# Kernel optimization log

Measured on AMD Instinct MI355X. Metric: run time of the kernel, lower is better.

Reference implementation:

```python
import jax, jax.numpy as jnp
import numpy as np

B, L, C, H, Wd = 256, 64, 256, 32, 32  # batch, num_filts, code_dim, height, width

def setup_inputs() -> dict:
    key = jax.random.key(0)
    k1, k2 = jax.random.split(key)
    code = jax.random.normal(k1, (B, L, C), dtype=jnp.float32)
    # stacked per-filter weights: weights[l].weight has shape [code_dim, H*W]
    W = jax.random.normal(k2, (L, C, H * Wd), dtype=jnp.float32) * (1.0 / np.sqrt(C))
    return {"code": code, "W": W}

def reference(code, W):
    # Original: for each filter l, x_hat[:, l] = code[:, l, :] @ weights[l].weight
    # (F.linear(x, weight.t()) == x @ weight). Fuse into one batched GEMM.
    # code: [B, L, C], W: [L, C, HW] -> out: [B, L, HW]
    x_hat = jnp.einsum('blc,lcd->bld', code, W)
    return x_hat.reshape(code.shape[0], W.shape[0], H, Wd)
```

## Files before the change

### kernel.cpp

```cpp
#include <hip/hip_runtime.h>
#include <hip/hip_bf16.h>

#define B_  256
#define L_  64
#define C_  256
#define HW_ 1024

typedef float  floatx4 __attribute__((ext_vector_type(4)));
typedef __bf16 bf16x8  __attribute__((ext_vector_type(8)));
typedef __bf16 bf16x4  __attribute__((ext_vector_type(4)));

#define LDT_A 72
#define LDB_ROW 128

#define BARRIER_LDS() asm volatile("s_waitcnt lgkmcnt(0)\n\ts_barrier" ::: "memory")

__device__ __forceinline__ int bswz(int n) { return (n ^ (n >> 2)) & 7; }

__global__ __launch_bounds__(512, 4)
void gld_mfma_kernel(const float* __restrict__ code,
                     const float* __restrict__ W,
                     float* __restrict__ out)
{
    const int tid = threadIdx.x;

    const int id  = blockIdx.x;
    const int ll  = id & 7;
    const int inr = id >> 3;
    const int m0  = (inr & 1) * 128;
    const int n0  = ((inr >> 1) & 7) * 128;
    const int l   = (inr >> 4) * 8 + ll;

    __shared__ __bf16 Alds[128 * LDT_A];
    __shared__ unsigned char Blds[128 * LDB_ROW];

    const int lane = tid & 63;
    const int wave = tid >> 6;
    const int wm = (wave >> 2) * 64;
    const int wn = (wave & 3) * 32;

    floatx4 acc[4][2];
    #pragma unroll
    for (int i = 0; i < 4; ++i)
        #pragma unroll
        for (int j = 0; j < 2; ++j)
            acc[i][j] = (floatx4)0.0f;

    const int a_row = tid >> 4;
    const int a_kc  = (tid & 15) * 4;
    const int b_i  = tid & 31;
    const int b_c8 = tid >> 5;

    const float* aBase = code + (size_t)m0 * (L_ * C_) + (size_t)l * C_ + a_kc;
    const float* wBase = W + (size_t)l * (C_ * HW_) + (size_t)(4 * b_c8) * HW_ + n0 + 4 * b_i;

    floatx4 Areg[2][4];
    floatx4 Breg[2][4];

    #pragma unroll
    for (int p = 0; p < 4; ++p)
        Areg[0][p] = *(const floatx4*)(aBase + (size_t)(p * 32 + a_row) * (L_ * C_));
    #pragma unroll
    for (int r = 0; r < 4; ++r)
        Breg[0][r] = *(const floatx4*)(wBase + (size_t)r * HW_);
    #pragma unroll
    for (int r = 0; r < 4; ++r)
        Breg[1][r] = *(const floatx4*)(wBase + (size_t)(64 + r) * HW_);

    int bwaddr[4];
    #pragma unroll
    for (int j = 0; j < 4; ++j) {
        const int row = 4 * b_i + j;
        bwaddr[j] = row * LDB_ROW + (((b_c8 >> 1) ^ bswz(row)) << 4) + ((b_c8 & 1) << 3);
    }

    #pragma unroll
    for (int kb = 0; kb < C_; kb += 64) {
        const int pp = (kb >> 6) & 1;

        if (kb + 64 < C_) {
            #pragma unroll
            for (int p = 0; p < 4; ++p)
                Areg[pp ^ 1][p] = *(const floatx4*)(aBase + (size_t)(p * 32 + a_row) * (L_ * C_) + (kb + 64));
        }

        #pragma unroll
        for (int j = 0; j < 4; ++j) {
            bf16x4 h;
            h.x = (__bf16)Breg[pp][0][j]; h.y = (__bf16)Breg[pp][1][j];
            h.z = (__bf16)Breg[pp][2][j]; h.w = (__bf16)Breg[pp][3][j];
            *(bf16x4*)&Blds[bwaddr[j]] = h;
        }

        if (kb + 128 < C_) {
            #pragma unroll
            for (int r = 0; r < 4; ++r)
                Breg[pp][r] = *(const floatx4*)(wBase + (size_t)(kb + 128 + r) * HW_);
        }

        #pragma unroll
        for (int p = 0; p < 4; ++p) {
            bf16x4 h;
            h.x = (__bf16)Areg[pp][p].x; h.y = (__bf16)Areg[pp][p].y;
            h.z = (__bf16)Areg[pp][p].z; h.w = (__bf16)Areg[pp][p].w;
            *(bf16x4*)&Alds[(p * 32 + a_row) * LDT_A + a_kc] = h;
        }

        BARRIER_LDS();

        #pragma unroll
        for (int ks = 0; ks < 2; ++ks) {
            bf16x8 af[4], bfr[2];
            const int koff = ks * 32 + (lane >> 4) * 8;
            #pragma unroll
            for (int i = 0; i < 4; ++i)
                af[i] = *(const bf16x8*)&Alds[(wm + i * 16 + (lane & 15)) * LDT_A + koff];
            #pragma unroll
            for (int j = 0; j < 2; ++j) {
                const int n = wn + j * 16 + (lane & 15);
                bfr[j] = *(const bf16x8*)&Blds[n * LDB_ROW + (((koff >> 3) ^ bswz(n)) << 4)];
            }
            #pragma unroll
            for (int i = 0; i < 4; ++i)
                #pragma unroll
                for (int j = 0; j < 2; ++j)
                    acc[i][j] = __builtin_amdgcn_mfma_f32_16x16x32_bf16(af[i], bfr[j], acc[i][j], 0, 0, 0);
        }

        BARRIER_LDS();
    }

    const int col0 = lane & 15;
    const int row0 = (lane >> 4) * 4;
    #pragma unroll
    for (int i = 0; i < 4; ++i) {
        #pragma unroll
        for (int j = 0; j < 2; ++j) {
            const int m = m0 + wm + i * 16 + row0;
            const int n = n0 + wn + j * 16 + col0;
            float* o = out + (size_t)m * (L_ * HW_) + (size_t)l * HW_ + n;
            #pragma unroll
            for (int r = 0; r < 4; ++r)
                o[(size_t)r * (L_ * HW_)] = acc[i][j][r];
        }
    }
}

extern "C" void kernel_launch(void* const* d_in, const int* in_sizes, int n_in,
                              void* d_out, int out_size, void* d_ws, size_t ws_size,
                              hipStream_t stream) {
    const float* code = (const float*)d_in[0];
    const float* W    = (const float*)d_in[1];
    float* out        = (float*)d_out;

    gld_mfma_kernel<<<dim3(1024), 512, 0, stream>>>(code, W, out);
}
```

Baseline: 132.4 us.

## Double-buffer LDS tiles and overlap MFMA compute with next-tile stores

Switches the A and B shared-memory tiles to two buffers. Each iteration now computes on the previous buffer while converting and writing the current tile into the other buffer, so only one barrier per k-step is needed instead of two. The B prefetch now runs one tile ahead instead of two, which lowers register pressure. In exchange LDS use doubles, and the bf16 conversions now share the instruction stream with the MFMAs.

```diff
diff --git a/kernel.cpp b/kernel.cpp
--- a/kernel.cpp
+++ b/kernel.cpp
@@ -17,6 +17,32 @@
 
 __device__ __forceinline__ int bswz(int n) { return (n ^ (n >> 2)) & 7; }
 
+
+__device__ __forceinline__ void compute_tile(const __bf16* __restrict__ Albuf,
+                                             const unsigned char* __restrict__ Blbuf,
+                                             floatx4 (&acc)[4][2],
+                                             int lane, int wm, int wn)
+{
+    #pragma unroll
+    for (int ks = 0; ks < 2; ++ks) {
+        bf16x8 af[4], bfr[2];
+        const int koff = ks * 32 + (lane >> 4) * 8;
+        #pragma unroll
+        for (int i = 0; i < 4; ++i)
+            af[i] = *(const bf16x8*)&Albuf[(wm + i * 16 + (lane & 15)) * LDT_A + koff];
+        #pragma unroll
+        for (int j = 0; j < 2; ++j) {
+            const int n = wn + j * 16 + (lane & 15);
+            bfr[j] = *(const bf16x8*)&Blbuf[n * LDB_ROW + (((koff >> 3) ^ bswz(n)) << 4)];
+        }
+        #pragma unroll
+        for (int i = 0; i < 4; ++i)
+            #pragma unroll
+            for (int j = 0; j < 2; ++j)
+                acc[i][j] = __builtin_amdgcn_mfma_f32_16x16x32_bf16(af[i], bfr[j], acc[i][j], 0, 0, 0);
+    }
+}
+
 __global__ __launch_bounds__(512, 4)
 void gld_mfma_kernel(const float* __restrict__ code,
                      const float* __restrict__ W,
@@ -31,8 +57,8 @@
     const int n0  = ((inr >> 1) & 7) * 128;
     const int l   = (inr >> 4) * 8 + ll;
 
-    __shared__ __bf16 Alds[128 * LDT_A];
-    __shared__ unsigned char Blds[128 * LDB_ROW];
+    __shared__ __bf16 Alds[2][128 * LDT_A];
+    __shared__ unsigned char Blds[2][128 * LDB_ROW];
 
     const int lane = tid & 63;
     const int wave = tid >> 6;
@@ -63,9 +89,6 @@
     #pragma unroll
     for (int r = 0; r < 4; ++r)
         Breg[0][r] = *(const floatx4*)(wBase + (size_t)r * HW_);
-    #pragma unroll
-    for (int r = 0; r < 4; ++r)
-        Breg[1][r] = *(const floatx4*)(wBase + (size_t)(64 + r) * HW_);
 
     int bwaddr[4];
     #pragma unroll
@@ -75,60 +98,41 @@
     }
 
     #pragma unroll
-    for (int kb = 0; kb < C_; kb += 64) {
-        const int pp = (kb >> 6) & 1;
+    for (int t = 0; t < 4; ++t) {
+        const int s  = t & 1;
+        const int kb = t * 64;
 
-        if (kb + 64 < C_) {
+        if (t < 3) {
             #pragma unroll
             for (int p = 0; p < 4; ++p)
-                Areg[pp ^ 1][p] = *(const floatx4*)(aBase + (size_t)(p * 32 + a_row) * (L_ * C_) + (kb + 64));
+                Areg[s ^ 1][p] = *(const floatx4*)(aBase + (size_t)(p * 32 + a_row) * (L_ * C_) + (kb + 64));
+            #pragma unroll
+            for (int r = 0; r < 4; ++r)
+                Breg[s ^ 1][r] = *(const floatx4*)(wBase + (size_t)(kb + 64 + r) * HW_);
         }
+
+        if (t > 0)
+            compute_tile(Alds[s ^ 1], Blds[s ^ 1], acc, lane, wm, wn);
 
         #pragma unroll
         for (int j = 0; j < 4; ++j) {
             bf16x4 h;
-            h.x = (__bf16)Breg[pp][0][j]; h.y = (__bf16)Breg[pp][1][j];
-            h.z = (__bf16)Breg[pp][2][j]; h.w = (__bf16)Breg[pp][3][j];
-            *(bf16x4*)&Blds[bwaddr[j]] = h;
+            h.x = (__bf16)Breg[s][0][j]; h.y = (__bf16)Breg[s][1][j];
+            h.z = (__bf16)Breg[s][2][j]; h.w = (__bf16)Breg[s][3][j];
+            *(bf16x4*)&Blds[s][bwaddr[j]] = h;
         }
-
-        if (kb + 128 < C_) {
-            #pragma unroll
-            for (int r = 0; r < 4; ++r)
-                Breg[pp][r] = *(const floatx4*)(wBase + (size_t)(kb + 128 + r) * HW_);
-        }
-
         #pragma unroll
         for (int p = 0; p < 4; ++p) {
             bf16x4 h;
-            h.x = (__bf16)Areg[pp][p].x; h.y = (__bf16)Areg[pp][p].y;
-            h.z = (__bf16)Areg[pp][p].z; h.w = (__bf16)Areg[pp][p].w;
-            *(bf16x4*)&Alds[(p * 32 + a_row) * LDT_A + a_kc] = h;
-        }
-
-        BARRIER_LDS();
-
-        #pragma unroll
-        for (int ks = 0; ks < 2; ++ks) {
-            bf16x8 af[4], bfr[2];
-            const int koff = ks * 32 + (lane >> 4) * 8;
-            #pragma unroll
-            for (int i = 0; i < 4; ++i)
-                af[i] = *(const bf16x8*)&Alds[(wm + i * 16 + (lane & 15)) * LDT_A + koff];
-            #pragma unroll
-            for (int j = 0; j < 2; ++j) {
-                const int n = wn + j * 16 + (lane & 15);
-                bfr[j] = *(const bf16x8*)&Blds[n * LDB_ROW + (((koff >> 3) ^ bswz(n)) << 4)];
-            }
-            #pragma unroll
-            for (int i = 0; i < 4; ++i)
-                #pragma unroll
-                for (int j = 0; j < 2; ++j)
-                    acc[i][j] = __builtin_amdgcn_mfma_f32_16x16x32_bf16(af[i], bfr[j], acc[i][j], 0, 0, 0);
+            h.x = (__bf16)Areg[s][p].x; h.y = (__bf16)Areg[s][p].y;
+            h.z = (__bf16)Areg[s][p].z; h.w = (__bf16)Areg[s][p].w;
+            *(bf16x4*)&Alds[s][(p * 32 + a_row) * LDT_A + a_kc] = h;
         }
 
         BARRIER_LDS();
     }
+
+    compute_tile(Alds[1], Blds[1], acc, lane, wm, wn);
 
     const int col0 = lane & 15;
     const int row0 = (lane >> 4) * 4;
```

Result: no change. 132.1 us (-0.2%).
